# Kernel tuning notes

Measured on AMD Instinct MI355X. Metric: run time of the kernel, lower is better.

The kernel has to match this reference:

```python
import jax, jax.numpy as jnp
import numpy as np

NNODES = 512   # sensors/nodes
WIN    = 64    # window_size (input features per node)
NH     = 64    # nhidden
NG     = 3     # ngnn iterations
BATCH  = 1024
OUT    = 32    # out_channels
EPS    = 1e-5  # BatchNorm1d eps


def setup_inputs() -> dict:
    key = jax.random.key(0)
    ks = jax.random.split(key, 8)
    X = jax.random.normal(ks[0], (BATCH, NNODES, WIN), jnp.float32)
    adj_const = jax.random.uniform(ks[1], (NNODES, NNODES), jnp.float32)
    # GCN layer 1 per gnn-iteration: window -> nhidden
    W1 = 0.05 * jax.random.normal(ks[2], (NG, WIN, NH), jnp.float32)
    b1 = jnp.zeros((NG, NH), jnp.float32)
    g1 = jnp.ones((NG, NNODES), jnp.float32)
    be1 = jnp.zeros((NG, NNODES), jnp.float32)
    # GCN layer 2 per gnn-iteration: nhidden -> nhidden
    W2 = 0.05 * jax.random.normal(ks[3], (NG, NH, NH), jnp.float32)
    b2 = jnp.zeros((NG, NH), jnp.float32)
    g2 = jnp.ones((NG, NNODES), jnp.float32)
    be2 = jnp.zeros((NG, NNODES), jnp.float32)
    Wfc = 0.05 * jax.random.normal(ks[4], (NG * NH, OUT), jnp.float32)
    bfc = jnp.zeros((OUT,), jnp.float32)
    return dict(X=X, adj_const=adj_const, W1=W1, b1=b1, g1=g1, be1=be1,
                W2=W2, b2=b2, g2=g2, be2=be2, Wfc=Wfc, bfc=bfc)


def _bn_nodes(h, gamma, beta):
    # torch BatchNorm1d(nnodes) on [B, N, F]: normalize per node channel over (B, F)
    mean = jnp.mean(h, axis=(0, 2), keepdims=True)
    var = jnp.var(h, axis=(0, 2), keepdims=True)
    return (h - mean) * jax.lax.rsqrt(var + EPS) * gamma[None, :, None] + beta[None, :, None]


def reference(X, adj_const, W1, b1, g1, be1, W2, b2, g2, be2, Wfc, bfc):
    # ConstantGraph returns the constant adjacency; z = ones - eye kills self-loops
    adj = adj_const * (1.0 - jnp.eye(NNODES, dtype=X.dtype))
    outs = []
    for i in range(NG):
        # GCNLayer: aggregate over neighbors then linear project
        h = jnp.einsum('nm,bmw->bnw', adj, X) @ W1[i] + b1[i]   # [B,N,NH]
        h = jax.nn.relu(h)
        h = _bn_nodes(h, g1[i], be1[i])
        skip = jnp.min(h, axis=1)                                # [B,NH]
        h = jnp.einsum('nm,bmd->bnd', adj, h) @ W2[i] + b2[i]
        h = jax.nn.relu(h)
        h = _bn_nodes(h, g2[i], be2[i])
        outs.append(jnp.min(h, axis=1) + skip)                   # [B,NH]
    h = jnp.concatenate(outs, axis=1)                            # [B, NG*NH]
    return h @ Wfc + bfc
```

## Files before the change

### kernel.cpp

```cpp
#include <hip/hip_runtime.h>


typedef short  s16x8 __attribute__((ext_vector_type(8)));
typedef float  f32x4 __attribute__((ext_vector_type(4)));

#define NN   512
#define NB   1024
#define NH   64
#define LDT  72

#define MFMA16(a, b, c) __builtin_amdgcn_mfma_f32_16x16x32_bf16((a), (b), (c), 0, 0, 0)

#define GLOAD16(g, l) __builtin_amdgcn_global_load_lds( \
    (const __attribute__((address_space(1))) unsigned*)(g), \
    (__attribute__((address_space(3))) unsigned*)(l), 16, 0, 0)

__device__ __forceinline__ unsigned short f2bf(float f) {
  union { float f; unsigned u; } v; v.f = f;
  unsigned r = v.u + 0x7fffu + ((v.u >> 16) & 1u);
  return (unsigned short)(r >> 16);
}
__device__ __forceinline__ float bf2f(unsigned short h) {
  union { unsigned u; float f; } v; v.u = ((unsigned)h) << 16;
  return v.f;
}

__global__ __launch_bounds__(256)
void k_prep(const float* __restrict__ X, const float* __restrict__ adj,
            const float* __restrict__ W1, const float* __restrict__ W2,
            unsigned short* __restrict__ Xt, unsigned short* __restrict__ adjbf,
            unsigned short* __restrict__ W1t, unsigned short* __restrict__ W2t) {
  __shared__ unsigned short T[64 * LDT];
  int blk = blockIdx.x, t = threadIdx.x;
  if (blk < 8192) {
    int b = blk >> 3, m0 = (blk & 7) << 6;
    int r = t >> 2, seg = t & 3;
    const float* src = X + ((size_t)b * NN + m0 + r) * NH + seg * 16;
#pragma unroll
    for (int e = 0; e < 16; ++e) T[(seg * 16 + e) * LDT + r] = f2bf(src[e]);
    __syncthreads();
    unsigned short* dst = Xt + ((size_t)b * NH + r) * NN + m0 + seg * 16;
    const unsigned short* sT = &T[r * LDT + seg * 16];
    *(s16x8*)dst       = *(const s16x8*)sT;
    *(s16x8*)(dst + 8) = *(const s16x8*)(sT + 8);
  } else if (blk < 9216) {
    int idx = (blk - 8192) * 256 + t;
    int n = idx >> 9, m = idx & 511;
    float v = adj[idx];
    if (n == m) v = 0.f;
    adjbf[idx] = f2bf(v);
  } else {
    int idx = (blk - 9216) * 256 + t;
    int i = idx >> 12, rc_ = idx & 4095;
    int src = (i << 12) + ((rc_ & 63) << 6) + (rc_ >> 6);
    W1t[idx] = f2bf(W1[src]);
    W2t[idx] = f2bf(W2[src]);
  }
}

__global__ __launch_bounds__(512)
void k_gnn1(const unsigned short* __restrict__ Xt, const unsigned short* __restrict__ adjbf,
            const unsigned short* __restrict__ W1t, const float* __restrict__ b1,
            unsigned short* __restrict__ H1T, float* __restrict__ SS1, float* __restrict__ SQ1) {
  __shared__ unsigned short Ab[2][2][4096];
  __shared__ unsigned short Bb[2][8192];
  int h = blockIdx.x;
  int blk = (h & 7) * 256 + (h >> 3);
  int bp = blk >> 2, n0 = (blk & 3) << 7;
  int b0 = bp * 2, b1v = bp * 2 + 1;
  int t = threadIdx.x, lane = t & 63, wid = t >> 6;
  int wf = wid & 1, wn = wid >> 1;
  int arow = wid * 8 + (lane >> 3);
  int swz = ((lane & 7) ^ (arow & 7)) << 3;
  const unsigned short* aS0 = Xt + ((size_t)b0  * NH + arow) * NN + swz;
  const unsigned short* aS1 = Xt + ((size_t)b1v * NH + arow) * NN + swz;
  const unsigned short* bS0 = adjbf + (size_t)(n0 + arow) * NN + swz;
  const unsigned short* bS1 = adjbf + (size_t)(n0 + 64 + arow) * NN + swz;

  GLOAD16(aS0, &Ab[0][0][wid * 512]);
  GLOAD16(aS1, &Ab[1][0][wid * 512]);
  GLOAD16(bS0, &Bb[0][wid * 512]);
  GLOAD16(bS1, &Bb[0][4096 + wid * 512]);
  __syncthreads();

  f32x4 acc[2][2][2] = {};
  for (int kt = 0; kt < 8; ++kt) {
    int cur = kt & 1;
    if (kt < 7) {
      int off = (kt + 1) * 64;
      GLOAD16(aS0 + off, &Ab[0][cur ^ 1][wid * 512]);
      GLOAD16(aS1 + off, &Ab[1][cur ^ 1][wid * 512]);
      GLOAD16(bS0 + off, &Bb[cur ^ 1][wid * 512]);
      GLOAD16(bS1 + off, &Bb[cur ^ 1][4096 + wid * 512]);
    }
    const unsigned short* B = Bb[cur];
#pragma unroll
    for (int kk = 0; kk < 2; ++kk) {
      int ks = (lane >> 4) + kk * 4;
      int ra0 = wf * 32 + (lane & 15), ra1 = ra0 + 16;
      int rb0 = wn * 32 + (lane & 15), rb1 = rb0 + 16;
      s16x8 bf0 = *(const s16x8*)&B[rb0 * 64 + ((ks ^ (rb0 & 7)) << 3)];
      s16x8 bf1 = *(const s16x8*)&B[rb1 * 64 + ((ks ^ (rb1 & 7)) << 3)];
#pragma unroll
      for (int bs = 0; bs < 2; ++bs) {
        const unsigned short* A = Ab[bs][cur];
        s16x8 a0 = *(const s16x8*)&A[ra0 * 64 + ((ks ^ (ra0 & 7)) << 3)];
        s16x8 a1 = *(const s16x8*)&A[ra1 * 64 + ((ks ^ (ra1 & 7)) << 3)];
        acc[bs][0][0] = MFMA16(a0, bf0, acc[bs][0][0]);
        acc[bs][1][0] = MFMA16(a1, bf0, acc[bs][1][0]);
        acc[bs][0][1] = MFMA16(a0, bf1, acc[bs][0][1]);
        acc[bs][1][1] = MFMA16(a1, bf1, acc[bs][1][1]);
      }
    }
    __syncthreads();
  }
#pragma unroll
  for (int bs = 0; bs < 2; ++bs) {
    unsigned short* T = Bb[bs];
#pragma unroll
    for (int fi = 0; fi < 2; ++fi)
#pragma unroll
      for (int fj = 0; fj < 2; ++fj) {
        int nl = wn * 32 + fj * 16 + (lane & 15);
        int w0 = wf * 32 + fi * 16 + (lane >> 4) * 4;
        ushort4 p;
        p.x = f2bf(acc[bs][fi][fj][0]); p.y = f2bf(acc[bs][fi][fj][1]);
        p.z = f2bf(acc[bs][fi][fj][2]); p.w = f2bf(acc[bs][fi][fj][3]);
        *(ushort4*)&T[nl * 64 + (((w0 >> 3) ^ (nl & 7)) << 3) + (w0 & 7)] = p;
      }
  }
#pragma unroll
  for (int j = 0; j < 3; ++j) {
    unsigned short* dstp = (j == 0) ? &Ab[0][0][wid * 512]
                         : (j == 1) ? &Ab[0][1][wid * 512] : &Ab[1][0][wid * 512];
    const unsigned short* gsrc = W1t + j * 4096 + (wid * 8 + (lane >> 3)) * 64
                               + (((lane & 7) ^ (lane >> 3)) << 3);
    GLOAD16(gsrc, dstp);
  }
  __syncthreads();
  int nrow = wid * 16 + (lane & 15);
  s16x8 aT[2][2];
#pragma unroll
  for (int bs = 0; bs < 2; ++bs)
#pragma unroll
    for (int kk = 0; kk < 2; ++kk) {
      int ks = (lane >> 4) + kk * 4;
      aT[bs][kk] = *(const s16x8*)&Bb[bs][nrow * 64 + ((ks ^ (nrow & 7)) << 3)];
    }
#pragma unroll
  for (int i = 0; i < 3; ++i) {
    const unsigned short* w1p = (i == 0) ? Ab[0][0] : (i == 1) ? Ab[0][1] : Ab[1][0];
    s16x8 bw[2][4];
#pragma unroll
    for (int kk = 0; kk < 2; ++kk) {
      int ks = (lane >> 4) + kk * 4;
#pragma unroll
      for (int fd = 0; fd < 4; ++fd) {
        int fr = fd * 16 + (lane & 15);
        bw[kk][fd] = *(const s16x8*)&w1p[fr * 64 + ((ks ^ (fr & 7)) << 3)];
      }
    }
    f32x4 acc2[2][4] = {};
#pragma unroll
    for (int bs = 0; bs < 2; ++bs)
#pragma unroll
      for (int kk = 0; kk < 2; ++kk) {
        acc2[bs][0] = MFMA16(aT[bs][kk], bw[kk][0], acc2[bs][0]);
        acc2[bs][1] = MFMA16(aT[bs][kk], bw[kk][1], acc2[bs][1]);
        acc2[bs][2] = MFMA16(aT[bs][kk], bw[kk][2], acc2[bs][2]);
        acc2[bs][3] = MFMA16(aT[bs][kk], bw[kk][3], acc2[bs][3]);
      }
    unsigned short* H1i = H1T + (size_t)i * 33554432u;
    float svr[4] = {0.f, 0.f, 0.f, 0.f}, sqr[4] = {0.f, 0.f, 0.f, 0.f};
#pragma unroll
    for (int bs = 0; bs < 2; ++bs) {
      int bcur = bs == 0 ? b0 : b1v;
#pragma unroll
      for (int fd = 0; fd < 4; ++fd) {
        int f = fd * 16 + (lane & 15);
        float bia = b1[i * 64 + f];
        float x0 = fmaxf(acc2[bs][fd][0] + bia, 0.f);
        float x1 = fmaxf(acc2[bs][fd][1] + bia, 0.f);
        float x2 = fmaxf(acc2[bs][fd][2] + bia, 0.f);
        float x3 = fmaxf(acc2[bs][fd][3] + bia, 0.f);
        svr[0] += x0; svr[1] += x1; svr[2] += x2; svr[3] += x3;
        sqr[0] += x0 * x0; sqr[1] += x1 * x1; sqr[2] += x2 * x2; sqr[3] += x3 * x3;
        ushort4 p;
        p.x = f2bf(x0); p.y = f2bf(x1); p.z = f2bf(x2); p.w = f2bf(x3);
        *(ushort4*)&H1i[((size_t)bcur * NH + f) * NN + n0 + wid * 16 + (lane >> 4) * 4] = p;
      }
    }
#pragma unroll
    for (int rr = 0; rr < 4; ++rr) {
      float sv = svr[rr], qv = sqr[rr];
      sv += __shfl_xor(sv, 1); sv += __shfl_xor(sv, 2); sv += __shfl_xor(sv, 4); sv += __shfl_xor(sv, 8);
      qv += __shfl_xor(qv, 1); qv += __shfl_xor(qv, 2); qv += __shfl_xor(qv, 4); qv += __shfl_xor(qv, 8);
      if ((lane & 15) == 0) {
        int n = n0 + wid * 16 + (lane >> 4) * 4 + rr;
        atomicAdd(&SS1[i * 512 + n], sv);
        atomicAdd(&SQ1[i * 512 + n], qv);
      }
    }
  }
}

__global__ __launch_bounds__(256)
void k_adjb_all(const unsigned short* __restrict__ adjbf,
                const float* __restrict__ SS1, const float* __restrict__ SQ1,
                const float* __restrict__ g1, const float* __restrict__ be1,
                unsigned short* __restrict__ ADJB3, float* __restrict__ RC3,
                float* __restrict__ A1, float* __restrict__ C1) {
  __shared__ float red[256];
  int blk = blockIdx.x;
  int i = blk >> 9, n = blk & 511, t = threadIdx.x;
  const float* Ssum = SS1 + i * 512;
  const float* Ssq  = SQ1 + i * 512;
  const float* g    = g1 + i * 512;
  const float* be   = be1 + i * 512;
  unsigned short* adjB = ADJB3 + (size_t)i * 262144;
  float acc = 0.f;
#pragma unroll
  for (int hh = 0; hh < 2; ++hh) {
    int m = t + hh * 256;
    float mean = Ssum[m] * (1.f / 65536.f);
    float var  = Ssq[m] * (1.f / 65536.f) - mean * mean;
    float a = g[m] * rsqrtf(var + 1e-5f);
    float c = be[m] - mean * a;
    if (n == 0) { A1[i * 512 + m] = a; C1[i * 512 + m] = c; }
    float av = bf2f(adjbf[n * NN + m]);
    adjB[n * NN + m] = f2bf(av * a);
    acc += av * c;
  }
  red[t] = acc; __syncthreads();
  for (int s = 128; s > 0; s >>= 1) { if (t < s) red[t] += red[t + s]; __syncthreads(); }
  if (t == 0) RC3[i * 512 + n] = red[0];
}

__global__ __launch_bounds__(256)
void k_minrow_all(const unsigned short* __restrict__ H2T0,
                  const unsigned short* __restrict__ H2T1,
                  const unsigned short* __restrict__ H2T2,
                  const float* __restrict__ SS2, const float* __restrict__ SQ2,
                  const float* __restrict__ g2, const float* __restrict__ be2,
                  const float* __restrict__ SKIP, float* __restrict__ outs) {
  int blk = blockIdx.x;
  int i = blk >> 14, rb = blk & 16383;
  const unsigned short* Ht = (i == 0) ? H2T0 : (i == 1) ? H2T1 : H2T2;
  const float* Ssum = SS2 + i * 512;
  const float* Ssq  = SQ2 + i * 512;
  const float* g    = g2 + i * 512;
  const float* be   = be2 + i * 512;
  const float* skip_i = SKIP + i * 65536;
  int t = threadIdx.x, lane = t & 63, wid = t >> 6;
  int row = rb * 4 + wid;
  int b = row >> 6, d = row & 63;
  s16x8 hv = *(const s16x8*)(Ht + (size_t)row * NN + lane * 8);
  float m = 1e30f;
#pragma unroll
  for (int e = 0; e < 8; ++e) {
    int mm = lane * 8 + e;
    float mean = Ssum[mm] * (1.f / 65536.f);
    float var  = Ssq[mm] * (1.f / 65536.f) - mean * mean;
    float a = g[mm] * rsqrtf(var + 1e-5f);
    float c = be[mm] - mean * a;
    m = fminf(m, a * bf2f((unsigned short)hv[e]) + c);
  }
#pragma unroll
  for (int off = 1; off < 64; off <<= 1) m = fminf(m, __shfl_xor(m, off));
  if (lane == 0) outs[(size_t)b * 192 + i * 64 + d] = m + skip_i[row];
}

__global__ __launch_bounds__(512)
void k_layer2(const unsigned short* __restrict__ H1T, const unsigned short* __restrict__ ADJB3,
              const float* __restrict__ RC3, const unsigned short* __restrict__ W2t,
              const float* __restrict__ b2,
              unsigned short* __restrict__ H2T0, unsigned short* __restrict__ H2T1,
              unsigned short* __restrict__ H2T2,
              float* __restrict__ SS2, float* __restrict__ SQ2,
              const float* __restrict__ A1, const float* __restrict__ C1,
              float* __restrict__ SKIP) {
  __shared__ unsigned short Ab[2][2][4096];
  __shared__ unsigned short Bb[2][8192];
  __shared__ float acs[512], ccs[512];
  int h = blockIdx.x;
  int blk = (h & 7) * 768 + (h >> 3);
  int i = blk / 2048;
  int r2 = blk - i * 2048;
  int bp = r2 >> 2, n0 = (r2 & 3) << 7;
  int b0 = bp * 2, b1v = bp * 2 + 1;
  const unsigned short* H1t_i = H1T + (size_t)i * 33554432u;
  const unsigned short* adjB  = ADJB3 + (size_t)i * 262144;
  const unsigned short* W2t_i = W2t + i * 4096;
  const float* rc  = RC3 + i * 512;
  const float* b2_i = b2 + i * 64;
  const float* A1v = A1 + i * 512;
  const float* C1v = C1 + i * 512;
  float* Ssum2 = SS2 + i * 512;
  float* Ssq2  = SQ2 + i * 512;
  float* skip_i = SKIP + i * 65536;
  unsigned short* H2t = (i == 0) ? H2T0 : (i == 1) ? H2T1 : H2T2;

  int t = threadIdx.x, lane = t & 63, wid = t >> 6;
  int wf = wid & 1, wn = wid >> 1;
  bool do_min = (n0 == 0);
  int arow = wid * 8 + (lane >> 3);
  int swz = ((lane & 7) ^ (arow & 7)) << 3;
  const unsigned short* aS0 = H1t_i + ((size_t)b0  * NH + arow) * NN + swz;
  const unsigned short* aS1 = H1t_i + ((size_t)b1v * NH + arow) * NN + swz;
  const unsigned short* bS0 = adjB + (size_t)(n0 + arow) * NN + swz;
  const unsigned short* bS1 = adjB + (size_t)(n0 + 64 + arow) * NN + swz;
  acs[t] = A1v[t]; ccs[t] = C1v[t];
  float rcv[2];
  rcv[0] = rc[n0 + wn * 32 + (lane & 15)];
  rcv[1] = rc[n0 + wn * 32 + 16 + (lane & 15)];

  GLOAD16(aS0, &Ab[0][0][wid * 512]);
  GLOAD16(aS1, &Ab[1][0][wid * 512]);
  GLOAD16(bS0, &Bb[0][wid * 512]);
  GLOAD16(bS1, &Bb[0][4096 + wid * 512]);
  __syncthreads();

  float mn0 = 1e30f, mn1 = 1e30f;
  f32x4 acc[2][2][2] = {};
  for (int kt = 0; kt < 8; ++kt) {
    int cur = kt & 1;
    if (kt < 7) {
      int off = (kt + 1) * 64;
      GLOAD16(aS0 + off, &Ab[0][cur ^ 1][wid * 512]);
      GLOAD16(aS1 + off, &Ab[1][cur ^ 1][wid * 512]);
      GLOAD16(bS0 + off, &Bb[cur ^ 1][wid * 512]);
      GLOAD16(bS1 + off, &Bb[cur ^ 1][4096 + wid * 512]);
    }
    if (do_min) {
      int s2 = ((lane & 7) ^ (arow & 7)) << 3;
      s16x8 av0 = *(const s16x8*)&Ab[0][cur][arow * 64 + s2];
      s16x8 av1 = *(const s16x8*)&Ab[1][cur][arow * 64 + s2];
      int m0 = kt * 64 + ((lane & 7) << 3);
#pragma unroll
      for (int e = 0; e < 8; ++e) {
        mn0 = fminf(mn0, acs[m0 + e] * bf2f((unsigned short)av0[e]) + ccs[m0 + e]);
        mn1 = fminf(mn1, acs[m0 + e] * bf2f((unsigned short)av1[e]) + ccs[m0 + e]);
      }
    }
    const unsigned short* B = Bb[cur];
#pragma unroll
    for (int kk = 0; kk < 2; ++kk) {
      int ks = (lane >> 4) + kk * 4;
      int ra0 = wf * 32 + (lane & 15), ra1 = ra0 + 16;
      int rb0 = wn * 32 + (lane & 15), rb1 = rb0 + 16;
      s16x8 bf0 = *(const s16x8*)&B[rb0 * 64 + ((ks ^ (rb0 & 7)) << 3)];
      s16x8 bf1 = *(const s16x8*)&B[rb1 * 64 + ((ks ^ (rb1 & 7)) << 3)];
#pragma unroll
      for (int bs = 0; bs < 2; ++bs) {
        const unsigned short* A = Ab[bs][cur];
        s16x8 a0 = *(const s16x8*)&A[ra0 * 64 + ((ks ^ (ra0 & 7)) << 3)];
        s16x8 a1 = *(const s16x8*)&A[ra1 * 64 + ((ks ^ (ra1 & 7)) << 3)];
        acc[bs][0][0] = MFMA16(a0, bf0, acc[bs][0][0]);
        acc[bs][1][0] = MFMA16(a1, bf0, acc[bs][1][0]);
        acc[bs][0][1] = MFMA16(a0, bf1, acc[bs][0][1]);
        acc[bs][1][1] = MFMA16(a1, bf1, acc[bs][1][1]);
      }
    }
    __syncthreads();
  }
  if (do_min) {
    mn0 = fminf(mn0, __shfl_xor(mn0, 1)); mn1 = fminf(mn1, __shfl_xor(mn1, 1));
    mn0 = fminf(mn0, __shfl_xor(mn0, 2)); mn1 = fminf(mn1, __shfl_xor(mn1, 2));
    mn0 = fminf(mn0, __shfl_xor(mn0, 4)); mn1 = fminf(mn1, __shfl_xor(mn1, 4));
    if ((lane & 7) == 0) {
      skip_i[b0 * 64 + arow] = mn0;
      skip_i[b1v * 64 + arow] = mn1;
    }
  }
#pragma unroll
  for (int bs = 0; bs < 2; ++bs) {
    unsigned short* Gt = Bb[bs];
#pragma unroll
    for (int fi = 0; fi < 2; ++fi)
#pragma unroll
      for (int fj = 0; fj < 2; ++fj) {
        int n  = wn * 32 + fj * 16 + (lane & 15);
        int f0 = wf * 32 + fi * 16 + (lane >> 4) * 4;
        ushort4 p;
        p.x = f2bf(acc[bs][fi][fj][0] + rcv[fj]); p.y = f2bf(acc[bs][fi][fj][1] + rcv[fj]);
        p.z = f2bf(acc[bs][fi][fj][2] + rcv[fj]); p.w = f2bf(acc[bs][fi][fj][3] + rcv[fj]);
        *(ushort4*)&Gt[n * 64 + (((f0 >> 3) ^ (n & 7)) << 3) + (f0 & 7)] = p;
      }
  }
  __syncthreads();
  s16x8 w2f[2][4];
  float bb[4];
#pragma unroll
  for (int kk = 0; kk < 2; ++kk)
#pragma unroll
    for (int fd = 0; fd < 4; ++fd)
      w2f[kk][fd] = *(const s16x8*)&W2t_i[(fd * 16 + (lane & 15)) * 64 + kk * 32 + (lane >> 4) * 8];
#pragma unroll
  for (int fd = 0; fd < 4; ++fd) bb[fd] = b2_i[fd * 16 + (lane & 15)];

  int nrow = wid * 16 + (lane & 15);
  f32x4 acc2[2][4] = {};
#pragma unroll
  for (int bs = 0; bs < 2; ++bs)
#pragma unroll
    for (int kk = 0; kk < 2; ++kk) {
      int ks = (lane >> 4) + kk * 4;
      s16x8 a = *(const s16x8*)&Bb[bs][nrow * 64 + ((ks ^ (nrow & 7)) << 3)];
      acc2[bs][0] = MFMA16(a, w2f[kk][0], acc2[bs][0]);
      acc2[bs][1] = MFMA16(a, w2f[kk][1], acc2[bs][1]);
      acc2[bs][2] = MFMA16(a, w2f[kk][2], acc2[bs][2]);
      acc2[bs][3] = MFMA16(a, w2f[kk][3], acc2[bs][3]);
    }
  float svr[4] = {0.f, 0.f, 0.f, 0.f}, sqr[4] = {0.f, 0.f, 0.f, 0.f};
#pragma unroll
  for (int bs = 0; bs < 2; ++bs) {
    int bcur = bs == 0 ? b0 : b1v;
#pragma unroll
    for (int fd = 0; fd < 4; ++fd) {
      int d  = fd * 16 + (lane & 15);
      int nw = n0 + wid * 16 + (lane >> 4) * 4;
      float x0 = fmaxf(acc2[bs][fd][0] + bb[fd], 0.f);
      float x1 = fmaxf(acc2[bs][fd][1] + bb[fd], 0.f);
      float x2 = fmaxf(acc2[bs][fd][2] + bb[fd], 0.f);
      float x3 = fmaxf(acc2[bs][fd][3] + bb[fd], 0.f);
      svr[0] += x0; svr[1] += x1; svr[2] += x2; svr[3] += x3;
      sqr[0] += x0 * x0; sqr[1] += x1 * x1; sqr[2] += x2 * x2; sqr[3] += x3 * x3;
      ushort4 p;
      p.x = f2bf(x0); p.y = f2bf(x1); p.z = f2bf(x2); p.w = f2bf(x3);
      *(ushort4*)&H2t[((size_t)bcur * NH + d) * NN + nw] = p;
    }
  }
#pragma unroll
  for (int rr = 0; rr < 4; ++rr) {
    float sv = svr[rr], qv = sqr[rr];
    sv += __shfl_xor(sv, 1); sv += __shfl_xor(sv, 2); sv += __shfl_xor(sv, 4); sv += __shfl_xor(sv, 8);
    qv += __shfl_xor(qv, 1); qv += __shfl_xor(qv, 2); qv += __shfl_xor(qv, 4); qv += __shfl_xor(qv, 8);
    if ((lane & 15) == 0) {
      int n = n0 + wid * 16 + (lane >> 4) * 4 + rr;
      atomicAdd(&Ssum2[n], sv);
      atomicAdd(&Ssq2[n], qv);
    }
  }
}

__global__ __launch_bounds__(256)
void k_fc(const float* __restrict__ outs, const float* __restrict__ Wfc,
          const float* __restrict__ bfc, float* __restrict__ out) {
  int t = threadIdx.x;
  int b = blockIdx.x * 8 + (t >> 5), o = t & 31;
  float acc = bfc[o];
  const float* orow = outs + (size_t)b * 192;
  for (int j = 0; j < 192; ++j) acc += orow[j] * Wfc[j * 32 + o];
  out[b * 32 + o] = acc;
}

extern "C" void kernel_launch(void* const* d_in, const int* in_sizes, int n_in,
                              void* d_out, int out_size, void* d_ws, size_t ws_size,
                              hipStream_t stream) {
  const float* X   = (const float*)d_in[0];
  const float* adj = (const float*)d_in[1];
  const float* W1  = (const float*)d_in[2];
  const float* b1  = (const float*)d_in[3];
  const float* g1  = (const float*)d_in[4];
  const float* be1 = (const float*)d_in[5];
  const float* W2  = (const float*)d_in[6];
  const float* b2  = (const float*)d_in[7];
  const float* g2  = (const float*)d_in[8];
  const float* be2 = (const float*)d_in[9];
  const float* Wfc = (const float*)d_in[10];
  const float* bfc = (const float*)d_in[11];
  float* out = (float*)d_out;

  char* ws = (char*)d_ws;
  size_t off = 0;
  auto alloc = [&](size_t bytes) {
    char* p = ws + off; off += (bytes + 255) & ~(size_t)255; return p;
  };
  unsigned short* ADJBF = (unsigned short*)alloc(512 * 512 * 2);
  unsigned short* ADJB3 = (unsigned short*)alloc((size_t)3 * 512 * 512 * 2);
  unsigned short* W1T   = (unsigned short*)alloc(3 * 4096 * 2);
  unsigned short* W2T   = (unsigned short*)alloc(3 * 4096 * 2);
  float* SS1 = (float*)alloc(3 * 512 * 4);
  float* SQ1 = (float*)alloc(3 * 512 * 4);
  float* SS2 = (float*)alloc(3 * 512 * 4);
  float* SQ2 = (float*)alloc(3 * 512 * 4);
  float* A1  = (float*)alloc(3 * 512 * 4);
  float* C1  = (float*)alloc(3 * 512 * 4);
  float* RC3 = (float*)alloc(3 * 512 * 4);
  float* SKIP = (float*)alloc(3 * 1024 * 64 * 4);
  float* OUTS = (float*)alloc(1024 * 192 * 4);
  unsigned short* XT   = (unsigned short*)alloc((size_t)1024 * 64 * 512 * 2);
  unsigned short* H1T  = (unsigned short*)alloc((size_t)3 * 1024 * 64 * 512 * 2);
  unsigned short* H2T1 = (unsigned short*)alloc((size_t)1024 * 64 * 512 * 2);
  unsigned short* H2T2 = (unsigned short*)alloc((size_t)1024 * 64 * 512 * 2);
  unsigned short* H2T0 = XT;

  hipMemsetAsync(SS1, 0, 4 * 3 * 512 * 4, stream);

  k_prep<<<9264, 256, 0, stream>>>(X, adj, W1, W2, XT, ADJBF, W1T, W2T);
  k_gnn1<<<2048, 512, 0, stream>>>(XT, ADJBF, W1T, b1, H1T, SS1, SQ1);
  k_adjb_all<<<1536, 256, 0, stream>>>(ADJBF, SS1, SQ1, g1, be1, ADJB3, RC3, A1, C1);
  k_layer2<<<6144, 512, 0, stream>>>(H1T, ADJB3, RC3, W2T, b2,
                                     H2T0, H2T1, H2T2, SS2, SQ2, A1, C1, SKIP);
  k_minrow_all<<<49152, 256, 0, stream>>>(H2T0, H2T1, H2T2, SS2, SQ2, g2, be2,
                                          SKIP, OUTS);
  k_fc<<<128, 256, 0, stream>>>(OUTS, Wfc, bfc, out);
}
```

Before: 485.6 us.

## Use single-buffered 128-wide K tiles in the adjacency GEMM loops

Both GEMM kernels (k_gnn1 and k_layer2) replace the double-buffered 64-wide K tiles with single-buffered 128-wide tiles. The loop drops from 8 steps to 4, and each stage loads two rows of 64 elements per 16-lane group with the same XOR swizzle. The aim is fewer loop iterations and barriers per block while keeping the LDS footprint the same. The cost is that global-to-LDS loads no longer overlap compute inside a block: each stage is loaded after the compute and a barrier, so latency hiding now relies on other resident blocks. As a small extra, the BN scale/shift table is only loaded into LDS by the blocks that compute the min.

```diff
diff --git a/kernel.cpp b/kernel.cpp
--- a/kernel.cpp
+++ b/kernel.cpp
@@ -62,50 +62,52 @@
 void k_gnn1(const unsigned short* __restrict__ Xt, const unsigned short* __restrict__ adjbf,
             const unsigned short* __restrict__ W1t, const float* __restrict__ b1,
             unsigned short* __restrict__ H1T, float* __restrict__ SS1, float* __restrict__ SQ1) {
-  __shared__ unsigned short Ab[2][2][4096];
-  __shared__ unsigned short Bb[2][8192];
+  __shared__ unsigned short Ab[2][8192];
+  __shared__ unsigned short Bb[16384];
   int h = blockIdx.x;
   int blk = (h & 7) * 256 + (h >> 3);
   int bp = blk >> 2, n0 = (blk & 3) << 7;
   int b0 = bp * 2, b1v = bp * 2 + 1;
   int t = threadIdx.x, lane = t & 63, wid = t >> 6;
   int wf = wid & 1, wn = wid >> 1;
-  int arow = wid * 8 + (lane >> 3);
-  int swz = ((lane & 7) ^ (arow & 7)) << 3;
-  const unsigned short* aS0 = Xt + ((size_t)b0  * NH + arow) * NN + swz;
-  const unsigned short* aS1 = Xt + ((size_t)b1v * NH + arow) * NN + swz;
-  const unsigned short* bS0 = adjbf + (size_t)(n0 + arow) * NN + swz;
-  const unsigned short* bS1 = adjbf + (size_t)(n0 + 64 + arow) * NN + swz;
-
-  GLOAD16(aS0, &Ab[0][0][wid * 512]);
-  GLOAD16(aS1, &Ab[1][0][wid * 512]);
-  GLOAD16(bS0, &Bb[0][wid * 512]);
-  GLOAD16(bS1, &Bb[0][4096 + wid * 512]);
+  const unsigned short* xb0 = Xt + (size_t)b0  * (NH * NN);
+  const unsigned short* xb1 = Xt + (size_t)b1v * (NH * NN);
+
+  auto stage = [&](int kt) {
+    int koff = kt * 128;
+    int sl = lane & 15;
+#pragma unroll
+    for (int q = 0; q < 2; ++q) {
+      int row = wid * 8 + q * 4 + (lane >> 4);
+      GLOAD16(xb0 + (size_t)row * NN + koff + ((sl ^ (row & 7)) << 3),
+              &Ab[0][(wid * 8 + q * 4) * 128]);
+      GLOAD16(xb1 + (size_t)row * NN + koff + ((sl ^ (row & 7)) << 3),
+              &Ab[1][(wid * 8 + q * 4) * 128]);
+    }
+#pragma unroll
+    for (int q = 0; q < 4; ++q) {
+      int row = wid * 16 + q * 4 + (lane >> 4);
+      GLOAD16(adjbf + (size_t)(n0 + row) * NN + koff + ((sl ^ (row & 7)) << 3),
+              &Bb[(wid * 16 + q * 4) * 128]);
+    }
+  };
+
+  stage(0);
   __syncthreads();
 
   f32x4 acc[2][2][2] = {};
-  for (int kt = 0; kt < 8; ++kt) {
-    int cur = kt & 1;
-    if (kt < 7) {
-      int off = (kt + 1) * 64;
-      GLOAD16(aS0 + off, &Ab[0][cur ^ 1][wid * 512]);
-      GLOAD16(aS1 + off, &Ab[1][cur ^ 1][wid * 512]);
-      GLOAD16(bS0 + off, &Bb[cur ^ 1][wid * 512]);
-      GLOAD16(bS1 + off, &Bb[cur ^ 1][4096 + wid * 512]);
-    }
-    const unsigned short* B = Bb[cur];
-#pragma unroll
-    for (int kk = 0; kk < 2; ++kk) {
+  for (int kt = 0; kt < 4; ++kt) {
+#pragma unroll
+    for (int kk = 0; kk < 4; ++kk) {
       int ks = (lane >> 4) + kk * 4;
       int ra0 = wf * 32 + (lane & 15), ra1 = ra0 + 16;
       int rb0 = wn * 32 + (lane & 15), rb1 = rb0 + 16;
-      s16x8 bf0 = *(const s16x8*)&B[rb0 * 64 + ((ks ^ (rb0 & 7)) << 3)];
-      s16x8 bf1 = *(const s16x8*)&B[rb1 * 64 + ((ks ^ (rb1 & 7)) << 3)];
+      s16x8 bf0 = *(const s16x8*)&Bb[rb0 * 128 + ((ks ^ (rb0 & 7)) << 3)];
+      s16x8 bf1 = *(const s16x8*)&Bb[rb1 * 128 + ((ks ^ (rb1 & 7)) << 3)];
 #pragma unroll
       for (int bs = 0; bs < 2; ++bs) {
-        const unsigned short* A = Ab[bs][cur];
-        s16x8 a0 = *(const s16x8*)&A[ra0 * 64 + ((ks ^ (ra0 & 7)) << 3)];
-        s16x8 a1 = *(const s16x8*)&A[ra1 * 64 + ((ks ^ (ra1 & 7)) << 3)];
+        s16x8 a0 = *(const s16x8*)&Ab[bs][ra0 * 128 + ((ks ^ (ra0 & 7)) << 3)];
+        s16x8 a1 = *(const s16x8*)&Ab[bs][ra1 * 128 + ((ks ^ (ra1 & 7)) << 3)];
         acc[bs][0][0] = MFMA16(a0, bf0, acc[bs][0][0]);
         acc[bs][1][0] = MFMA16(a1, bf0, acc[bs][1][0]);
         acc[bs][0][1] = MFMA16(a0, bf1, acc[bs][0][1]);
@@ -113,10 +115,14 @@
       }
     }
     __syncthreads();
+    if (kt < 3) {
+      stage(kt + 1);
+      __syncthreads();
+    }
   }
 #pragma unroll
   for (int bs = 0; bs < 2; ++bs) {
-    unsigned short* T = Bb[bs];
+    unsigned short* T = &Bb[bs * 8192];
 #pragma unroll
     for (int fi = 0; fi < 2; ++fi)
 #pragma unroll
@@ -131,8 +137,8 @@
   }
 #pragma unroll
   for (int j = 0; j < 3; ++j) {
-    unsigned short* dstp = (j == 0) ? &Ab[0][0][wid * 512]
-                         : (j == 1) ? &Ab[0][1][wid * 512] : &Ab[1][0][wid * 512];
+    unsigned short* dstp = (j == 0) ? &Ab[0][wid * 512]
+                         : (j == 1) ? &Ab[0][4096 + wid * 512] : &Ab[1][wid * 512];
     const unsigned short* gsrc = W1t + j * 4096 + (wid * 8 + (lane >> 3)) * 64
                                + (((lane & 7) ^ (lane >> 3)) << 3);
     GLOAD16(gsrc, dstp);
@@ -145,11 +151,11 @@
 #pragma unroll
     for (int kk = 0; kk < 2; ++kk) {
       int ks = (lane >> 4) + kk * 4;
-      aT[bs][kk] = *(const s16x8*)&Bb[bs][nrow * 64 + ((ks ^ (nrow & 7)) << 3)];
+      aT[bs][kk] = *(const s16x8*)&Bb[bs * 8192 + nrow * 64 + ((ks ^ (nrow & 7)) << 3)];
     }
 #pragma unroll
   for (int i = 0; i < 3; ++i) {
-    const unsigned short* w1p = (i == 0) ? Ab[0][0] : (i == 1) ? Ab[0][1] : Ab[1][0];
+    const unsigned short* w1p = (i == 0) ? &Ab[0][0] : (i == 1) ? &Ab[0][4096] : &Ab[1][0];
     s16x8 bw[2][4];
 #pragma unroll
     for (int kk = 0; kk < 2; ++kk) {
@@ -279,8 +285,8 @@
               float* __restrict__ SS2, float* __restrict__ SQ2,
               const float* __restrict__ A1, const float* __restrict__ C1,
               float* __restrict__ SKIP) {
-  __shared__ unsigned short Ab[2][2][4096];
-  __shared__ unsigned short Bb[2][8192];
+  __shared__ unsigned short Ab[2][8192];
+  __shared__ unsigned short Bb[16384];
   __shared__ float acs[512], ccs[512];
   int h = blockIdx.x;
   int blk = (h & 7) * 768 + (h >> 3);
@@ -304,57 +310,64 @@
   int wf = wid & 1, wn = wid >> 1;
   bool do_min = (n0 == 0);
   int arow = wid * 8 + (lane >> 3);
-  int swz = ((lane & 7) ^ (arow & 7)) << 3;
-  const unsigned short* aS0 = H1t_i + ((size_t)b0  * NH + arow) * NN + swz;
-  const unsigned short* aS1 = H1t_i + ((size_t)b1v * NH + arow) * NN + swz;
-  const unsigned short* bS0 = adjB + (size_t)(n0 + arow) * NN + swz;
-  const unsigned short* bS1 = adjB + (size_t)(n0 + 64 + arow) * NN + swz;
-  acs[t] = A1v[t]; ccs[t] = C1v[t];
+  const unsigned short* hb0 = H1t_i + (size_t)b0  * (NH * NN);
+  const unsigned short* hb1 = H1t_i + (size_t)b1v * (NH * NN);
+  if (do_min) { acs[t] = A1v[t]; ccs[t] = C1v[t]; }
   float rcv[2];
   rcv[0] = rc[n0 + wn * 32 + (lane & 15)];
   rcv[1] = rc[n0 + wn * 32 + 16 + (lane & 15)];
 
-  GLOAD16(aS0, &Ab[0][0][wid * 512]);
-  GLOAD16(aS1, &Ab[1][0][wid * 512]);
-  GLOAD16(bS0, &Bb[0][wid * 512]);
-  GLOAD16(bS1, &Bb[0][4096 + wid * 512]);
+  auto stage = [&](int kt) {
+    int koff = kt * 128;
+    int sl = lane & 15;
+#pragma unroll
+    for (int q = 0; q < 2; ++q) {
+      int row = wid * 8 + q * 4 + (lane >> 4);
+      GLOAD16(hb0 + (size_t)row * NN + koff + ((sl ^ (row & 7)) << 3),
+              &Ab[0][(wid * 8 + q * 4) * 128]);
+      GLOAD16(hb1 + (size_t)row * NN + koff + ((sl ^ (row & 7)) << 3),
+              &Ab[1][(wid * 8 + q * 4) * 128]);
+    }
+#pragma unroll
+    for (int q = 0; q < 4; ++q) {
+      int row = wid * 16 + q * 4 + (lane >> 4);
+      GLOAD16(adjB + (size_t)(n0 + row) * NN + koff + ((sl ^ (row & 7)) << 3),
+              &Bb[(wid * 16 + q * 4) * 128]);
+    }
+  };
+
+  stage(0);
   __syncthreads();
 
   float mn0 = 1e30f, mn1 = 1e30f;
   f32x4 acc[2][2][2] = {};
-  for (int kt = 0; kt < 8; ++kt) {
-    int cur = kt & 1;
-    if (kt < 7) {
-      int off = (kt + 1) * 64;
-      GLOAD16(aS0 + off, &Ab[0][cur ^ 1][wid * 512]);
-      GLOAD16(aS1 + off, &Ab[1][cur ^ 1][wid * 512]);
-      GLOAD16(bS0 + off, &Bb[cur ^ 1][wid * 512]);
-      GLOAD16(bS1 + off, &Bb[cur ^ 1][4096 + wid * 512]);
-    }
+  for (int kt = 0; kt < 4; ++kt) {
     if (do_min) {
-      int s2 = ((lane & 7) ^ (arow & 7)) << 3;
-      s16x8 av0 = *(const s16x8*)&Ab[0][cur][arow * 64 + s2];
-      s16x8 av1 = *(const s16x8*)&Ab[1][cur][arow * 64 + s2];
-      int m0 = kt * 64 + ((lane & 7) << 3);
-#pragma unroll
-      for (int e = 0; e < 8; ++e) {
-        mn0 = fminf(mn0, acs[m0 + e] * bf2f((unsigned short)av0[e]) + ccs[m0 + e]);
-        mn1 = fminf(mn1, acs[m0 + e] * bf2f((unsigned short)av1[e]) + ccs[m0 + e]);
-      }
-    }
-    const unsigned short* B = Bb[cur];
-#pragma unroll
-    for (int kk = 0; kk < 2; ++kk) {
+#pragma unroll
+      for (int half = 0; half < 2; ++half) {
+        int sl = (lane & 7) + half * 8;
+        int so = (sl ^ (arow & 7)) << 3;
+        s16x8 av0 = *(const s16x8*)&Ab[0][arow * 128 + so];
+        s16x8 av1 = *(const s16x8*)&Ab[1][arow * 128 + so];
+        int m0 = kt * 128 + sl * 8;
+#pragma unroll
+        for (int e = 0; e < 8; ++e) {
+          mn0 = fminf(mn0, acs[m0 + e] * bf2f((unsigned short)av0[e]) + ccs[m0 + e]);
+          mn1 = fminf(mn1, acs[m0 + e] * bf2f((unsigned short)av1[e]) + ccs[m0 + e]);
+        }
+      }
+    }
+#pragma unroll
+    for (int kk = 0; kk < 4; ++kk) {
       int ks = (lane >> 4) + kk * 4;
       int ra0 = wf * 32 + (lane & 15), ra1 = ra0 + 16;
       int rb0 = wn * 32 + (lane & 15), rb1 = rb0 + 16;
-      s16x8 bf0 = *(const s16x8*)&B[rb0 * 64 + ((ks ^ (rb0 & 7)) << 3)];
-      s16x8 bf1 = *(const s16x8*)&B[rb1 * 64 + ((ks ^ (rb1 & 7)) << 3)];
+      s16x8 bf0 = *(const s16x8*)&Bb[rb0 * 128 + ((ks ^ (rb0 & 7)) << 3)];
+      s16x8 bf1 = *(const s16x8*)&Bb[rb1 * 128 + ((ks ^ (rb1 & 7)) << 3)];
 #pragma unroll
       for (int bs = 0; bs < 2; ++bs) {
-        const unsigned short* A = Ab[bs][cur];
-        s16x8 a0 = *(const s16x8*)&A[ra0 * 64 + ((ks ^ (ra0 & 7)) << 3)];
-        s16x8 a1 = *(const s16x8*)&A[ra1 * 64 + ((ks ^ (ra1 & 7)) << 3)];
+        s16x8 a0 = *(const s16x8*)&Ab[bs][ra0 * 128 + ((ks ^ (ra0 & 7)) << 3)];
+        s16x8 a1 = *(const s16x8*)&Ab[bs][ra1 * 128 + ((ks ^ (ra1 & 7)) << 3)];
         acc[bs][0][0] = MFMA16(a0, bf0, acc[bs][0][0]);
         acc[bs][1][0] = MFMA16(a1, bf0, acc[bs][1][0]);
         acc[bs][0][1] = MFMA16(a0, bf1, acc[bs][0][1]);
@@ -362,6 +375,10 @@
       }
     }
     __syncthreads();
+    if (kt < 3) {
+      stage(kt + 1);
+      __syncthreads();
+    }
   }
   if (do_min) {
     mn0 = fminf(mn0, __shfl_xor(mn0, 1)); mn1 = fminf(mn1, __shfl_xor(mn1, 1));
@@ -374,7 +391,7 @@
   }
 #pragma unroll
   for (int bs = 0; bs < 2; ++bs) {
-    unsigned short* Gt = Bb[bs];
+    unsigned short* Gt = &Bb[bs * 8192];
 #pragma unroll
     for (int fi = 0; fi < 2; ++fi)
 #pragma unroll
@@ -405,7 +422,7 @@
 #pragma unroll
     for (int kk = 0; kk < 2; ++kk) {
       int ks = (lane >> 4) + kk * 4;
-      s16x8 a = *(const s16x8*)&Bb[bs][nrow * 64 + ((ks ^ (nrow & 7)) << 3)];
+      s16x8 a = *(const s16x8*)&Bb[bs * 8192 + nrow * 64 + ((ks ^ (nrow & 7)) << 3)];
       acc2[bs][0] = MFMA16(a, w2f[kk][0], acc2[bs][0]);
       acc2[bs][1] = MFMA16(a, w2f[kk][1], acc2[bs][1]);
       acc2[bs][2] = MFMA16(a, w2f[kk][2], acc2[bs][2]);
```

After: 497.5 us. 1.02x slower.
